# Optimization experiments

Measured on AMD Instinct MI355X. Metric: run time of the kernel, lower is better.

## Reference

```python
import jax, jax.numpy as jnp
import numpy as np
import math

B, N, D, H, K = 8, 256, 128, 256, 128


def setup_inputs() -> dict:
    key = jax.random.key(0)
    ks = jax.random.split(key, 8)
    # forward args
    x = jax.random.uniform(ks[0], (B, N, N), dtype=jnp.float32) * 3.0  # pairwise distances
    atom_embeds = jax.random.normal(ks[1], (B, N, D), dtype=jnp.float32)
    # params of nn.Linear(2D, H) and nn.Linear(H, 2) (store as [in, out])
    lim1 = 1.0 / math.sqrt(2 * D)
    W1 = jax.random.uniform(ks[2], (2 * D, H), minval=-lim1, maxval=lim1, dtype=jnp.float32)
    b1 = jax.random.uniform(ks[3], (H,), minval=-lim1, maxval=lim1, dtype=jnp.float32)
    lim2 = 1.0 / math.sqrt(H)
    W2 = jax.random.uniform(ks[4], (H, 2), minval=-lim2, maxval=lim2, dtype=jnp.float32)
    b2 = jax.random.uniform(ks[5], (2,), minval=-lim2, maxval=lim2, dtype=jnp.float32)
    # RBF params: means ~ U(0,3), temps ~ U(0.1,10)
    means = jax.random.uniform(ks[6], (K,), minval=0.0, maxval=3.0, dtype=jnp.float32)
    temps = jax.random.uniform(ks[7], (K,), minval=0.1, maxval=10.0, dtype=jnp.float32)
    return {"x": x, "atom_embeds": atom_embeds, "W1": W1, "b1": b1,
            "W2": W2, "b2": b2, "means": means, "temps": temps}


def reference(x, atom_embeds, W1, b1, W2, b2, means, temps):
    d = atom_embeds.shape[-1]
    scale = 1.0 / math.sqrt(2 * d)
    # Split-weight trick: cat([e_i, e_j]) @ W1 == e_i @ W1[:D] + e_j @ W1[D:]
    # (same math, avoids materializing the [B,N,N,2D] concat)
    hi = jnp.einsum('bnd,dh->bnh', atom_embeds, W1[:d])   # [B,N,H]
    hj = jnp.einsum('bnd,dh->bnh', atom_embeds, W1[d:])   # [B,N,H]
    h = jax.nn.relu(hi[:, :, None, :] + hj[:, None, :, :] + b1)  # [B,N,N,H]
    edge_features = (jnp.einsum('bijh,ho->bijo', h, W2) + b2) * scale  # [B,N,N,2]
    mul = edge_features[..., 0:1]   # [B,N,N,1]
    bias = edge_features[..., 1:2]  # [B,N,N,1]
    v = mul * x[..., None] + bias   # [B,N,N,1]
    temp = jnp.abs(temps)
    # RBF gaussian basis expansion -> [B,N,N,K]
    return jnp.exp(-jnp.square(v - means) * temp)
```

## Files before the change

kernel.cpp:

```cpp
#include <hip/hip_runtime.h>
#include <hip/hip_bf16.h>


#define NB 8
#define NN 256
#define ND 128
#define NH 256
#define NK 128
#define GI 4

typedef float f32x4 __attribute__((ext_vector_type(4)));

__global__ __launch_bounds__(256) void precompute_hij(
    const float* __restrict__ atom, const float* __restrict__ W1,
    const float* __restrict__ b1,
    float* __restrict__ hi, float* __restrict__ hjbT) {
  const int h = threadIdx.x;
  const int base = blockIdx.x * 8;
  const int b  = base >> 8;
  const int j0 = base & 255;
  __shared__ float a[8][ND];
  for (int t = threadIdx.x; t < 8 * ND; t += 256) {
    a[t >> 7][t & 127] = atom[(size_t)base * ND + t];
  }
  __syncthreads();
  float acc0[8], acc1[8];
  const float bv = b1[h];
#pragma unroll
  for (int r = 0; r < 8; ++r) { acc0[r] = 0.f; acc1[r] = bv; }
  for (int d = 0; d < ND; ++d) {
    const float w0 = W1[d * NH + h];
    const float w1 = W1[(ND + d) * NH + h];
#pragma unroll
    for (int r = 0; r < 8; ++r) {
      acc0[r] = fmaf(a[r][d], w0, acc0[r]);
      acc1[r] = fmaf(a[r][d], w1, acc1[r]);
    }
  }
#pragma unroll
  for (int r = 0; r < 8; ++r) {
    hi[(size_t)(base + r) * NH + h] = acc0[r];
    hjbT[((size_t)b * NH + h) * NN + (j0 + r)] = acc1[r];
  }
}

__global__ __launch_bounds__(256) void edge_rbf(
    const float* __restrict__ x,
    const float* __restrict__ hi, const float* __restrict__ hjbT,
    const float* __restrict__ W2, const float* __restrict__ b2,
    const float* __restrict__ means, const float* __restrict__ temps,
    float* __restrict__ out) {
  const int b    = blockIdx.x & 7;
  const int i0   = (blockIdx.x >> 3) * GI;
  const int tid  = threadIdx.x;
  const int lane = tid & 63;
  const int wv   = __builtin_amdgcn_readfirstlane(tid >> 6);

  __shared__ float part0[4][GI][NN];
  __shared__ float part1[4][GI][NN];
  __shared__ float vsh[GI][NN];

  const float* __restrict__ hjrow  = hjbT + ((size_t)b * NH + wv * 64) * NN + 4 * lane;
  const float* __restrict__ w2row  = W2 + wv * 128;
  const float* __restrict__ hibase = hi + ((size_t)(b * NN + i0)) * NH + wv * 64;

  float acc0[GI][4], acc1[GI][4];
#pragma unroll
  for (int r = 0; r < GI; ++r)
#pragma unroll
    for (int q = 0; q < 4; ++q) { acc0[r][q] = 0.f; acc1[r][q] = 0.f; }

#pragma unroll 8
  for (int hh = 0; hh < 64; ++hh) {
    const float4 hj4 = *reinterpret_cast<const float4*>(hjrow + (size_t)hh * NN);
    const float w0 = w2row[2 * hh];
    const float w1 = w2row[2 * hh + 1];
#pragma unroll
    for (int r = 0; r < GI; ++r) {
      const float hih = hibase[(size_t)r * NH + hh];
      const float a0 = fmaxf(hih + hj4.x, 0.f);
      const float a1 = fmaxf(hih + hj4.y, 0.f);
      const float a2 = fmaxf(hih + hj4.z, 0.f);
      const float a3 = fmaxf(hih + hj4.w, 0.f);
      acc0[r][0] = fmaf(a0, w0, acc0[r][0]); acc1[r][0] = fmaf(a0, w1, acc1[r][0]);
      acc0[r][1] = fmaf(a1, w0, acc0[r][1]); acc1[r][1] = fmaf(a1, w1, acc1[r][1]);
      acc0[r][2] = fmaf(a2, w0, acc0[r][2]); acc1[r][2] = fmaf(a2, w1, acc1[r][2]);
      acc0[r][3] = fmaf(a3, w0, acc0[r][3]); acc1[r][3] = fmaf(a3, w1, acc1[r][3]);
    }
  }
#pragma unroll
  for (int r = 0; r < GI; ++r) {
    *reinterpret_cast<float4*>(&part0[wv][r][4 * lane]) =
        make_float4(acc0[r][0], acc0[r][1], acc0[r][2], acc0[r][3]);
    *reinterpret_cast<float4*>(&part1[wv][r][4 * lane]) =
        make_float4(acc1[r][0], acc1[r][1], acc1[r][2], acc1[r][3]);
  }
  __syncthreads();

  {
    const float scale = 0.0625f;
    const float b20 = b2[0], b21 = b2[1];
#pragma unroll
    for (int r = 0; r < GI; ++r) {
      const float s0 = part0[0][r][tid] + part0[1][r][tid] + part0[2][r][tid] + part0[3][r][tid];
      const float s1 = part1[0][r][tid] + part1[1][r][tid] + part1[2][r][tid] + part1[3][r][tid];
      const float mul  = (s0 + b20) * scale;
      const float bias = (s1 + b21) * scale;
      vsh[r][tid] = fmaf(mul, x[(size_t)(b * NN + i0 + r) * NN + tid], bias);
    }
  }
  __syncthreads();

  const int k0 = (lane & 31) * 4;
  const int jhalf = lane >> 5;
  const float LOG2E = 1.44269504088896340736f;
  const float4 mv = *reinterpret_cast<const float4*>(means + k0);
  const float4 tl = *reinterpret_cast<const float4*>(temps + k0);
  const float t0 = -fabsf(tl.x) * LOG2E;
  const float t1 = -fabsf(tl.y) * LOG2E;
  const float t2 = -fabsf(tl.z) * LOG2E;
  const float t3 = -fabsf(tl.w) * LOG2E;

#pragma unroll
  for (int r = 0; r < GI; ++r) {
    float* __restrict__ orow = out + ((size_t)(b * NN + i0 + r) * NN + wv * 64) * NK;
#pragma unroll 4
    for (int c = 0; c < 32; ++c) {
      const int j = 2 * c + jhalf;
      const float vj = vsh[r][wv * 64 + j];
      const float d0 = vj - mv.x;
      const float d1 = vj - mv.y;
      const float d2 = vj - mv.z;
      const float d3 = vj - mv.w;
      f32x4 e;
      e.x = __builtin_amdgcn_exp2f(d0 * d0 * t0);
      e.y = __builtin_amdgcn_exp2f(d1 * d1 * t1);
      e.z = __builtin_amdgcn_exp2f(d2 * d2 * t2);
      e.w = __builtin_amdgcn_exp2f(d3 * d3 * t3);
      *reinterpret_cast<f32x4*>(orow + (size_t)j * NK + k0) = e;
    }
  }
}

extern "C" void kernel_launch(void* const* d_in, const int* in_sizes, int n_in,
                              void* d_out, int out_size, void* d_ws, size_t ws_size,
                              hipStream_t stream) {
  const float* x     = (const float*)d_in[0];
  const float* atom  = (const float*)d_in[1];
  const float* W1    = (const float*)d_in[2];
  const float* b1    = (const float*)d_in[3];
  const float* W2    = (const float*)d_in[4];
  const float* b2    = (const float*)d_in[5];
  const float* means = (const float*)d_in[6];
  const float* temps = (const float*)d_in[7];
  float* out = (float*)d_out;

  float* hi   = (float*)d_ws;
  float* hjbT = hi + (size_t)NB * NN * NH;

  precompute_hij<<<NB * NN / 8, 256, 0, stream>>>(atom, W1, b1, hi, hjbT);
  edge_rbf<<<NB * NN / GI, 256, 0, stream>>>(x, hi, hjbT, W2, b2, means, temps, out);
}
```

Measured before the change: 80.81 us.

## Split edge kernel across 8 waves with fewer rows and LDS-staged weights

Result: faster. 74.15 us (-8.2%).

```diff
diff --git a/kernel.cpp b/kernel.cpp
--- a/kernel.cpp
+++ b/kernel.cpp
@@ -7,9 +7,10 @@
 #define ND 128
 #define NH 256
 #define NK 128
-#define GI 4
+#define GI 2
 
 typedef float f32x4 __attribute__((ext_vector_type(4)));
+typedef float f32x2 __attribute__((ext_vector_type(2)));
 
 __global__ __launch_bounds__(256) void precompute_hij(
     const float* __restrict__ atom, const float* __restrict__ W1,
@@ -44,7 +45,7 @@
   }
 }
 
-__global__ __launch_bounds__(256) void edge_rbf(
+__global__ __launch_bounds__(512, 8) void edge_rbf(
     const float* __restrict__ x,
     const float* __restrict__ hi, const float* __restrict__ hjbT,
     const float* __restrict__ W2, const float* __restrict__ b2,
@@ -54,15 +55,23 @@
   const int i0   = (blockIdx.x >> 3) * GI;
   const int tid  = threadIdx.x;
   const int lane = tid & 63;
-  const int wv   = __builtin_amdgcn_readfirstlane(tid >> 6);
+  const int wv   = tid >> 6;
 
-  __shared__ float part0[4][GI][NN];
-  __shared__ float part1[4][GI][NN];
+  __shared__ float part0[8][GI][NN];
+  __shared__ float part1[8][GI][NN];
+  __shared__ float hi_lds[GI][NH];
+  __shared__ f32x2 w2_lds[NH];
   __shared__ float vsh[GI][NN];
 
-  const float* __restrict__ hjrow  = hjbT + ((size_t)b * NH + wv * 64) * NN + 4 * lane;
-  const float* __restrict__ w2row  = W2 + wv * 128;
-  const float* __restrict__ hibase = hi + ((size_t)(b * NN + i0)) * NH + wv * 64;
+  {
+    hi_lds[tid >> 8][tid & 255] = hi[((size_t)(b * NN + i0)) * NH + tid];
+    if (tid < NH) {
+      w2_lds[tid] = *reinterpret_cast<const f32x2*>(W2 + 2 * tid);
+    }
+  }
+  __syncthreads();
+
+  const float* __restrict__ hjrow = hjbT + ((size_t)b * NH + wv * 32) * NN + 4 * lane;
 
   float acc0[GI][4], acc1[GI][4];
 #pragma unroll
@@ -71,21 +80,21 @@
     for (int q = 0; q < 4; ++q) { acc0[r][q] = 0.f; acc1[r][q] = 0.f; }
 
 #pragma unroll 8
-  for (int hh = 0; hh < 64; ++hh) {
+  for (int hh = 0; hh < 32; ++hh) {
+    const int h = wv * 32 + hh;
     const float4 hj4 = *reinterpret_cast<const float4*>(hjrow + (size_t)hh * NN);
-    const float w0 = w2row[2 * hh];
-    const float w1 = w2row[2 * hh + 1];
+    const f32x2 w = w2_lds[h];
 #pragma unroll
     for (int r = 0; r < GI; ++r) {
-      const float hih = hibase[(size_t)r * NH + hh];
+      const float hih = hi_lds[r][h];
       const float a0 = fmaxf(hih + hj4.x, 0.f);
       const float a1 = fmaxf(hih + hj4.y, 0.f);
       const float a2 = fmaxf(hih + hj4.z, 0.f);
       const float a3 = fmaxf(hih + hj4.w, 0.f);
-      acc0[r][0] = fmaf(a0, w0, acc0[r][0]); acc1[r][0] = fmaf(a0, w1, acc1[r][0]);
-      acc0[r][1] = fmaf(a1, w0, acc0[r][1]); acc1[r][1] = fmaf(a1, w1, acc1[r][1]);
-      acc0[r][2] = fmaf(a2, w0, acc0[r][2]); acc1[r][2] = fmaf(a2, w1, acc1[r][2]);
-      acc0[r][3] = fmaf(a3, w0, acc0[r][3]); acc1[r][3] = fmaf(a3, w1, acc1[r][3]);
+      acc0[r][0] = fmaf(a0, w.x, acc0[r][0]); acc1[r][0] = fmaf(a0, w.y, acc1[r][0]);
+      acc0[r][1] = fmaf(a1, w.x, acc0[r][1]); acc1[r][1] = fmaf(a1, w.y, acc1[r][1]);
+      acc0[r][2] = fmaf(a2, w.x, acc0[r][2]); acc1[r][2] = fmaf(a2, w.y, acc1[r][2]);
+      acc0[r][3] = fmaf(a3, w.x, acc0[r][3]); acc1[r][3] = fmaf(a3, w.y, acc1[r][3]);
     }
   }
 #pragma unroll
@@ -98,16 +107,15 @@
   __syncthreads();
 
   {
+    const int r = tid >> 8;
+    const int j = tid & 255;
+    float s0 = 0.f, s1 = 0.f;
+#pragma unroll
+    for (int w = 0; w < 8; ++w) { s0 += part0[w][r][j]; s1 += part1[w][r][j]; }
     const float scale = 0.0625f;
-    const float b20 = b2[0], b21 = b2[1];
-#pragma unroll
-    for (int r = 0; r < GI; ++r) {
-      const float s0 = part0[0][r][tid] + part0[1][r][tid] + part0[2][r][tid] + part0[3][r][tid];
-      const float s1 = part1[0][r][tid] + part1[1][r][tid] + part1[2][r][tid] + part1[3][r][tid];
-      const float mul  = (s0 + b20) * scale;
-      const float bias = (s1 + b21) * scale;
-      vsh[r][tid] = fmaf(mul, x[(size_t)(b * NN + i0 + r) * NN + tid], bias);
-    }
+    const float mul  = (s0 + b2[0]) * scale;
+    const float bias = (s1 + b2[1]) * scale;
+    vsh[r][j] = fmaf(mul, x[(size_t)(b * NN + i0 + r) * NN + j], bias);
   }
   __syncthreads();
 
@@ -123,11 +131,11 @@
 
 #pragma unroll
   for (int r = 0; r < GI; ++r) {
-    float* __restrict__ orow = out + ((size_t)(b * NN + i0 + r) * NN + wv * 64) * NK;
+    float* __restrict__ orow = out + ((size_t)(b * NN + i0 + r) * NN + wv * 32) * NK;
 #pragma unroll 4
-    for (int c = 0; c < 32; ++c) {
+    for (int c = 0; c < 16; ++c) {
       const int j = 2 * c + jhalf;
-      const float vj = vsh[r][wv * 64 + j];
+      const float vj = vsh[r][wv * 32 + j];
       const float d0 = vj - mv.x;
       const float d1 = vj - mv.y;
       const float d2 = vj - mv.z;
@@ -159,5 +167,5 @@
   float* hjbT = hi + (size_t)NB * NN * NH;
 
   precompute_hij<<<NB * NN / 8, 256, 0, stream>>>(atom, W1, b1, hi, hjbT);
-  edge_rbf<<<NB * NN / GI, 256, 0, stream>>>(x, hi, hjbT, W2, b2, means, temps, out);
+  edge_rbf<<<NB * NN / GI, 512, 0, stream>>>(x, hi, hjbT, W2, b2, means, temps, out);
 }
```
